# Performance work log

Hardware: AMD Instinct MI355X
Metric: run time of the kernel (lower is better)

The kernel has to match this reference:

```python
import jax, jax.numpy as jnp
import numpy as np

N, E, D, H = 16000, 256000, 128, 4
ALPHA = 0.2  # LeakyReLU negative slope


def setup_inputs() -> dict:
    key = jax.random.key(0)
    ks = jax.random.split(key, 9)
    s = 0.1
    return {
        "h": jax.random.normal(ks[0], (N, D), jnp.float32),
        "W": jax.random.normal(ks[1], (H, D, D), jnp.float32) * s,
        "a": jax.random.normal(ks[2], (H, 2 * D), jnp.float32) * s,
        "W_ih": jax.random.normal(ks[3], (3 * D, H * D), jnp.float32) * s,
        "W_hh": jax.random.normal(ks[4], (3 * D, D), jnp.float32) * s,
        "b_ih": jnp.zeros((3 * D,), jnp.float32),
        "b_hh": jnp.zeros((3 * D,), jnp.float32),
        "src": jax.random.randint(ks[5], (E,), 0, N, jnp.int32),
        "dst": jax.random.randint(ks[6], (E,), 0, N, jnp.int32),
    }


def reference(h, W, a, W_ih, W_hh, b_ih, b_hh, src, dst):
    n = h.shape[0]
    # Per-head linear transform: Wh[n,h,d]
    Wh = jnp.einsum("nd,hde->nhe", h, W)
    a1, a2 = a[:, :D], a[:, D:]
    s_src = jnp.einsum("nhd,hd->nh", Wh, a1)  # src attention logits
    s_dst = jnp.einsum("nhd,hd->nh", Wh, a2)  # dst attention logits
    e = jax.nn.leaky_relu(s_src[src] + s_dst[dst], ALPHA)  # [E,H]
    # Segment softmax over incoming edges of each dst node
    m = jax.ops.segment_max(e, dst, num_segments=n)          # [N,H]
    ex = jnp.exp(e - m[dst])
    denom = jax.ops.segment_sum(ex, dst, num_segments=n)     # [N,H]
    att = ex / denom[dst]                                    # [E,H]
    # Weighted message aggregation: h_prime[n,h,d]
    h_prime = jax.ops.segment_sum(att[:, :, None] * Wh[src], dst, num_segments=n)
    x = h_prime.reshape(n, H * D)  # concat heads
    # PyTorch GRUCell(input=H*D, hidden=D)
    gi = x @ W_ih.T + b_ih
    gh = h @ W_hh.T + b_hh
    i_r, i_z, i_n = jnp.split(gi, 3, axis=1)
    h_r, h_z, h_n = jnp.split(gh, 3, axis=1)
    r = jax.nn.sigmoid(i_r + h_r)
    z = jax.nn.sigmoid(i_z + h_z)
    nvec = jnp.tanh(i_n + r * h_n)
    return (1.0 - z) * nvec + z * h
```

## Files before the change

### kernel.cpp

```cpp
#include <hip/hip_runtime.h>
#include <math.h>

#define N_NODES 16000
#define E_EDGES 256000
#define DIM 128
#define HEADS 4
#define LRELU_ALPHA 0.2f
#define SLOT 64

typedef unsigned short u16;
typedef unsigned int u32;
typedef short bf16x8 __attribute__((ext_vector_type(8)));
typedef float floatx4 __attribute__((ext_vector_type(4)));

#define AS1 __attribute__((address_space(1)))
#define AS3 __attribute__((address_space(3)))

__device__ __forceinline__ u16 f2bf(float f) {
    u32 u = __float_as_uint(f);
    u32 r = (u + 0x7fffu + ((u >> 16) & 1u)) >> 16;
    return (u16)r;
}
__device__ __forceinline__ float bflo(u32 v) { return __uint_as_float(v << 16); }
__device__ __forceinline__ float bfhi(u32 v) { return __uint_as_float(v & 0xffff0000u); }
__device__ __forceinline__ u32 pack2(float lo, float hi) {
    return (u32)f2bf(lo) | ((u32)f2bf(hi) << 16);
}

__global__ __launch_bounds__(256) void prep_kernel(
    const float* __restrict__ W, const float* __restrict__ a,
    const float* __restrict__ W_ih, const float* __restrict__ W_hh,
    const int* __restrict__ src, const int* __restrict__ dst,
    u16* __restrict__ Wihb, u16* __restrict__ Wb,
    u16* __restrict__ Wcat, float* __restrict__ wa1, float* __restrict__ wa2,
    u32* __restrict__ cnt, int* __restrict__ ssort)
{
    const int b = blockIdx.x;
    const int tid = threadIdx.x;
    if (b < 1000) {
        int e = b * 256 + tid;
        u32 base = cnt[N_NODES];
        int d = dst[e];
        u32 pos = atomicAdd(&cnt[d], 1u) - base;
        ssort[d * SLOT + pos] = src[e];
    } else if (b < 1768) {
        int i = (b - 1000) * 256 + tid;
        Wihb[i] = f2bf(W_ih[i]);
        if (i < HEADS * DIM * DIM) Wb[i] = f2bf(W[i]);
    } else if (b < 1960) {
        int t = (b - 1768) * 256 + tid;
        int jp = t >> 7, e = t & 127;
        int j = (jp < 256) ? jp : jp + 128;
        Wcat[(size_t)j * 640 + 512 + e] = f2bf(W_hh[jp * 128 + e]);
    } else {
        int t = (b - 1960) * 256 + tid;
        int h = t >> 7;
        const float* wrow = W + (long)t * DIM;
        const float* a1 = a + h * 2 * DIM;
        const float* a2 = a1 + DIM;
        float s1 = 0.f, s2 = 0.f;
        for (int e = 0; e < DIM; ++e) {
            float w = wrow[e];
            s1 = fmaf(w, a1[e], s1);
            s2 = fmaf(w, a2[e], s2);
        }
        wa1[t] = s1;
        wa2[t] = s2;
    }
}

__device__ __forceinline__ void score_wave(int n, const float* __restrict__ hin,
    const float* __restrict__ wa1, const float* __restrict__ wa2,
    float* __restrict__ s_src, float* __restrict__ s_dst, u16* __restrict__ xcat, int lane)
{
    float2 hv = ((const float2*)hin)[n * 64 + lane];
    ((u32*)xcat)[n * 320 + 256 + lane] = pack2(hv.x, hv.y);
    float ps[4], qs[4];
    #pragma unroll
    for (int h = 0; h < 4; ++h) {
        float2 w1 = ((const float2*)(wa1 + h * 128))[lane];
        float2 w2 = ((const float2*)(wa2 + h * 128))[lane];
        float p = hv.x * w1.x + hv.y * w1.y;
        float q = hv.x * w2.x + hv.y * w2.y;
        #pragma unroll
        for (int off = 32; off > 0; off >>= 1) {
            p += __shfl_xor(p, off, 64);
            q += __shfl_xor(q, off, 64);
        }
        ps[h] = p; qs[h] = q;
    }
    if (lane == 0) {
        #pragma unroll
        for (int h = 0; h < 4; ++h) {
            s_src[n * HEADS + h] = ps[h];
            s_dst[n * HEADS + h] = qs[h];
        }
    }
}

__device__ __forceinline__ void gemm_tile(const u16* A, const u16* Bt, u16* C,
    int kstart, int kend, int lda, int ldb, int ldc, int row0, int col0, char* SMp, int tid)
{
    u16 (*Alds)[32] = (u16(*)[32])SMp;
    u16 (*Blds)[32] = (u16(*)[32])(SMp + 8192);
    const int wave = tid >> 6;
    const int lane = tid & 63;
    const int quad = lane >> 4;
    const int l15  = lane & 15;
    const int wm = (wave >> 1) * 64;
    const int wn = (wave & 1) * 64;
    const int ch0 = wave * 2;
    const int srow = lane >> 2;
    const int scol = (lane & 3) * 8;

    floatx4 acc[4][4] = {};

    for (int k0 = kstart; k0 < kend; k0 += 32) {
        #pragma unroll
        for (int c = 0; c < 2; ++c) {
            int ch = ch0 + c;
            const u16* ga = A + (size_t)(row0 + ch * 16 + srow) * lda + k0 + scol;
            __builtin_amdgcn_global_load_lds((AS1 void*)ga, (AS3 void*)&Alds[ch * 16][0], 16, 0, 0);
            const u16* gb = Bt + (size_t)(col0 + ch * 16 + srow) * ldb + k0 + scol;
            __builtin_amdgcn_global_load_lds((AS1 void*)gb, (AS3 void*)&Blds[ch * 16][0], 16, 0, 0);
        }
        __syncthreads();
        bf16x8 af[4], bfr[4];
        #pragma unroll
        for (int i = 0; i < 4; ++i) af[i] = *(const bf16x8*)&Alds[wm + i * 16 + l15][quad * 8];
        #pragma unroll
        for (int j = 0; j < 4; ++j) bfr[j] = *(const bf16x8*)&Blds[wn + j * 16 + l15][quad * 8];
        #pragma unroll
        for (int i = 0; i < 4; ++i)
            #pragma unroll
            for (int j = 0; j < 4; ++j)
                acc[i][j] = __builtin_amdgcn_mfma_f32_16x16x32_bf16(af[i], bfr[j], acc[i][j], 0, 0, 0);
        __syncthreads();
    }
    #pragma unroll
    for (int i = 0; i < 4; ++i) {
        #pragma unroll
        for (int r = 0; r < 4; ++r) {
            int row = row0 + wm + i * 16 + quad * 4 + r;
            size_t base = (size_t)row * ldc + col0 + wn + l15;
            #pragma unroll
            for (int j = 0; j < 4; ++j) C[base + j * 16] = f2bf(acc[i][j][r]);
        }
    }
}

__global__ __launch_bounds__(256) void mt_scores_kernel(
    const u16* __restrict__ Wihb, const u16* __restrict__ Wb, u16* __restrict__ Wcat,
    const float* __restrict__ hin, const float* __restrict__ wa1, const float* __restrict__ wa2,
    float* __restrict__ s_src, float* __restrict__ s_dst, u16* __restrict__ xcat)
{
    __shared__ __align__(16) char SM[16384];
    const int tid = threadIdx.x;
    const int b = blockIdx.x;
    if (b < 12) {
        int y = b % 3, z = b / 3;
        gemm_tile(Wihb + z * 128, Wb + (size_t)z * 16384, Wcat + z * 128,
                  0, 128, 512, 128, 640, y * 128, 0, SM, tid);
    } else {
        for (int n = (b - 12) * 4 + (tid >> 6); n < N_NODES; n += 1024 * 4)
            score_wave(n, hin, wa1, wa2, s_src, s_dst, xcat, tid & 63);
    }
}

__global__ __launch_bounds__(256) void aggregate_kernel(
    const float* __restrict__ s_src, const float* __restrict__ s_dst,
    const u32* __restrict__ cnt, const int* __restrict__ srcs,
    u16* __restrict__ xcat)
{
    const int tid = threadIdx.x;
    const int lane = tid & 63;
    const int n = blockIdx.x * 4 + (tid >> 6);
    const u32 base = cnt[N_NODES];
    const int deg = (int)(cnt[n] - base);
    const int start = n * SLOT;
    u32* xrow = (u32*)(xcat + (size_t)n * 640);
    if (deg == 0) {
        #pragma unroll
        for (int h = 0; h < 4; ++h) xrow[h * 64 + lane] = 0u;
        return;
    }
    const u32* hb = (const u32*)xcat;
    const float sd = s_dst[n * HEADS + (lane & 3)];
    const int j16 = lane >> 2;
    const int hh  = lane & 3;

    float2 acc[4] = {{0.f,0.f},{0.f,0.f},{0.f,0.f},{0.f,0.f}};
    float dsum[4] = {0.f, 0.f, 0.f, 0.f};

    for (int cb = 0; cb < deg; cb += 16) {
        const int clen = min(16, deg - cb);
        int sv = 0;
        if (lane < clen) sv = srcs[start + cb + lane];
        float wv = 0.f;
        if (j16 < clen) {
            int s = __shfl(sv, j16, 64);
            float e = s_src[s * HEADS + hh] + sd;
            e = e > 0.f ? e : LRELU_ALPHA * e;
            wv = __expf(e);
        }
        int e = 0;
        for (; e + 8 <= clen; e += 8) {
            u32 vs[8];
            #pragma unroll
            for (int k = 0; k < 8; ++k) {
                int s = __shfl(sv, e + k, 64);
                vs[k] = hb[s * 320 + 256 + lane];
            }
            #pragma unroll
            for (int k = 0; k < 8; ++k) {
                float lo = bflo(vs[k]), hi = bfhi(vs[k]);
                #pragma unroll
                for (int h = 0; h < 4; ++h) {
                    float w = __shfl(wv, (e + k) * 4 + h, 64);
                    acc[h].x = fmaf(w, lo, acc[h].x);
                    acc[h].y = fmaf(w, hi, acc[h].y);
                    dsum[h] += w;
                }
            }
        }
        for (; e < clen; ++e) {
            int s = __shfl(sv, e, 64);
            u32 v = hb[s * 320 + 256 + lane];
            float lo = bflo(v), hi = bfhi(v);
            #pragma unroll
            for (int h = 0; h < 4; ++h) {
                float w = __shfl(wv, e * 4 + h, 64);
                acc[h].x = fmaf(w, lo, acc[h].x);
                acc[h].y = fmaf(w, hi, acc[h].y);
                dsum[h] += w;
            }
        }
    }
    #pragma unroll
    for (int h = 0; h < 4; ++h) {
        float invd = 1.f / dsum[h];
        xrow[h * 64 + lane] = pack2(acc[h].x * invd, acc[h].y * invd);
    }
}

__global__ __launch_bounds__(256) void gemm_main_kernel(
    const u16* __restrict__ xcat, const u16* __restrict__ Wcat, u16* __restrict__ g)
{
    __shared__ __align__(16) char SM[16384];
    const int x = blockIdx.x;
    const int ks0 = (x == 3) ? 512 : 0;
    const int ke0 = (x == 2) ? 512 : 640;
    const int mid = (ks0 + ke0) >> 1;
    const int ks = blockIdx.z ? mid : ks0;
    const int ke = blockIdx.z ? ke0 : mid;
    u16* gp = g + (size_t)blockIdx.z * N_NODES * 512;
    gemm_tile(xcat, Wcat, gp, ks, ke, 640, 640, 512,
              blockIdx.y * 128, x * 128, SM, threadIdx.x);
}

__global__ __launch_bounds__(256) void gru_kernel(const u32* __restrict__ g32,
    const float* __restrict__ b_ih, const float* __restrict__ b_hh,
    const float* __restrict__ hin, float* __restrict__ out)
{
    int p = blockIdx.x * 256 + threadIdx.x;
    if (p >= N_NODES * 64) return;
    int n = p >> 6, d2 = p & 63;
    const u32* gr0 = g32 + (size_t)n * 256;
    const u32* gr1 = gr0 + (size_t)N_NODES * 256;
    u32 ar = gr0[d2],       br = gr1[d2];
    u32 az = gr0[64 + d2],  bz = gr1[64 + d2];
    u32 ai = gr0[128 + d2], bi = gr1[128 + d2];
    u32 ah = gr0[192 + d2], bh = gr1[192 + d2];
    const float2* bi2 = (const float2*)b_ih;
    const float2* bh2 = (const float2*)b_hh;
    float2 bir = bi2[d2],       bhr = bh2[d2];
    float2 biz = bi2[64 + d2],  bhz = bh2[64 + d2];
    float2 bin = bi2[128 + d2], bhn = bh2[128 + d2];
    float2 hv = ((const float2*)hin)[p];
    float2 o;
    {
        float A = bflo(ar) + bflo(br) + bir.x + bhr.x;
        float B = bflo(az) + bflo(bz) + biz.x + bhz.x;
        float Cn = bflo(ai) + bflo(bi) + bin.x;
        float Dn = bflo(ah) + bflo(bh) + bhn.x;
        float r = 1.f / (1.f + __expf(-A));
        float z = 1.f / (1.f + __expf(-B));
        float e2 = __expf(2.f * (Cn + r * Dn));
        float nv = (e2 - 1.f) / (e2 + 1.f);
        o.x = (1.f - z) * nv + z * hv.x;
    }
    {
        float A = bfhi(ar) + bfhi(br) + bir.y + bhr.y;
        float B = bfhi(az) + bfhi(bz) + biz.y + bhz.y;
        float Cn = bfhi(ai) + bfhi(bi) + bin.y;
        float Dn = bfhi(ah) + bfhi(bh) + bhn.y;
        float r = 1.f / (1.f + __expf(-A));
        float z = 1.f / (1.f + __expf(-B));
        float e2 = __expf(2.f * (Cn + r * Dn));
        float nv = (e2 - 1.f) / (e2 + 1.f);
        o.y = (1.f - z) * nv + z * hv.y;
    }
    ((float2*)out)[p] = o;
}

extern "C" void kernel_launch(void* const* d_in, const int* in_sizes, int n_in,
                              void* d_out, int out_size, void* d_ws, size_t ws_size,
                              hipStream_t stream)
{
    const float* h    = (const float*)d_in[0];
    const float* W    = (const float*)d_in[1];
    const float* a    = (const float*)d_in[2];
    const float* W_ih = (const float*)d_in[3];
    const float* W_hh = (const float*)d_in[4];
    const float* b_ih = (const float*)d_in[5];
    const float* b_hh = (const float*)d_in[6];
    const int*   src  = (const int*)d_in[7];
    const int*   dst  = (const int*)d_in[8];
    float* out = (float*)d_out;

    char* ws = (char*)d_ws;
    size_t off = 0;
    auto alloc = [&](size_t bytes) { void* p = ws + off; off += (bytes + 255) & ~(size_t)255; return p; };

    u16*   xcat = (u16*)alloc((size_t)N_NODES * 640 * 2);
    u16*   g    = (u16*)alloc((size_t)N_NODES * 512 * 2 * 2);
    u16*   Wihb = (u16*)alloc(384 * 512 * 2);
    u16*   Wb   = (u16*)alloc(HEADS * DIM * DIM * 2);
    u16*   Wcat = (u16*)alloc(512 * 640 * 2);
    float* wa1  = (float*)alloc(512 * 4);
    float* wa2  = (float*)alloc(512 * 4);
    float* s_src = (float*)alloc((size_t)N_NODES * HEADS * 4);
    float* s_dst = (float*)alloc((size_t)N_NODES * HEADS * 4);
    u32*   cnt  = (u32*)alloc((N_NODES + 1) * 4);
    int*   ssort = (int*)alloc((size_t)N_NODES * SLOT * 4);

    prep_kernel<<<1962, 256, 0, stream>>>(
        W, a, W_ih, W_hh, src, dst, Wihb, Wb, Wcat, wa1, wa2, cnt, ssort);

    mt_scores_kernel<<<1036, 256, 0, stream>>>(
        Wihb, Wb, Wcat, h, wa1, wa2, s_src, s_dst, xcat);

    aggregate_kernel<<<N_NODES / 4, 256, 0, stream>>>(s_src, s_dst, cnt, ssort, xcat);

    gemm_main_kernel<<<dim3(4, 125, 2), 256, 0, stream>>>(xcat, Wcat, g);

    gru_kernel<<<(N_NODES * 64 + 255) / 256, 256, 0, stream>>>(
        (const u32*)g, b_ih, b_hh, h, out);
}
```

Before: 153.4 us.

## Fuse final GEMM with GRU epilogue via gate-interleaved weight layout

Reorders the output columns of the concatenated weight so that each 128-column tile holds the r, z, i_n and h_n gates for 32 hidden dims, interleaved. The combined r/z gate sums now accumulate in a single K=640 pass, with zeroed blocks keeping the n-gate input and hidden parts separate. The GEMM is then fused with the GRU nonlinearity through an LDS-staged epilogue. This removes the bf16 intermediate g buffer (two split-K halves), its write and re-read, and one kernel launch. In exchange the grid drops from 1000 to 500 blocks, each doing the full K loop, and the output stores are 4-byte per thread.

```diff
diff --git a/kernel.cpp b/kernel.cpp
--- a/kernel.cpp
+++ b/kernel.cpp
@@ -23,9 +23,11 @@
 }
 __device__ __forceinline__ float bflo(u32 v) { return __uint_as_float(v << 16); }
 __device__ __forceinline__ float bfhi(u32 v) { return __uint_as_float(v & 0xffff0000u); }
+__device__ __forceinline__ float bfs(u16 v) { return __uint_as_float((u32)v << 16); }
 __device__ __forceinline__ u32 pack2(float lo, float hi) {
     return (u32)f2bf(lo) | ((u32)f2bf(hi) << 16);
 }
+
 
 __global__ __launch_bounds__(256) void prep_kernel(
     const float* __restrict__ W, const float* __restrict__ a,
@@ -50,10 +52,22 @@
     } else if (b < 1960) {
         int t = (b - 1768) * 256 + tid;
         int jp = t >> 7, e = t & 127;
-        int j = (jp < 256) ? jp : jp + 128;
-        Wcat[(size_t)j * 640 + 512 + e] = f2bf(W_hh[jp * 128 + e]);
+        int gate = jp >> 7;
+        if (gate == 2) gate = 3;
+        int p = (jp & 127) * 4 + gate;
+        Wcat[(size_t)p * 640 + 512 + e] = f2bf(W_hh[jp * 128 + e]);
+    } else if (b < 2280) {
+        int t = (b - 1960) * 256 + tid;
+        if (t < 16384) {
+            int d = t >> 7, e = t & 127;
+            Wcat[(size_t)(d * 4 + 2) * 640 + 512 + e] = 0;
+        } else {
+            int t2 = t - 16384;
+            int d = t2 >> 9, c = t2 & 511;
+            Wcat[(size_t)(d * 4 + 3) * 640 + c] = 0;
+        }
     } else {
-        int t = (b - 1960) * 256 + tid;
+        int t = (b - 2280) * 256 + tid;
         int h = t >> 7;
         const float* wrow = W + (long)t * DIM;
         const float* a1 = a + h * 2 * DIM;
@@ -98,6 +112,7 @@
     }
 }
 
+template<int PERM_C>
 __device__ __forceinline__ void gemm_tile(const u16* A, const u16* Bt, u16* C,
     int kstart, int kend, int lda, int ldb, int ldc, int row0, int col0, char* SMp, int tid)
 {
@@ -142,6 +157,7 @@
         #pragma unroll
         for (int r = 0; r < 4; ++r) {
             int row = row0 + wm + i * 16 + quad * 4 + r;
+            if (PERM_C) row = (row & 127) * 4 + (row >> 7);
             size_t base = (size_t)row * ldc + col0 + wn + l15;
             #pragma unroll
             for (int j = 0; j < 4; ++j) C[base + j * 16] = f2bf(acc[i][j][r]);
@@ -159,8 +175,8 @@
     const int b = blockIdx.x;
     if (b < 12) {
         int y = b % 3, z = b / 3;
-        gemm_tile(Wihb + z * 128, Wb + (size_t)z * 16384, Wcat + z * 128,
-                  0, 128, 512, 128, 640, y * 128, 0, SM, tid);
+        gemm_tile<1>(Wihb + z * 128, Wb + (size_t)z * 16384, Wcat + z * 128,
+                     0, 128, 512, 128, 640, y * 128, 0, SM, tid);
     } else {
         for (int n = (b - 12) * 4 + (tid >> 6); n < N_NODES; n += 1024 * 4)
             score_wave(n, hin, wa1, wa2, s_src, s_dst, xcat, tid & 63);
@@ -243,64 +259,83 @@
     }
 }
 
-__global__ __launch_bounds__(256) void gemm_main_kernel(
-    const u16* __restrict__ xcat, const u16* __restrict__ Wcat, u16* __restrict__ g)
-{
-    __shared__ __align__(16) char SM[16384];
-    const int x = blockIdx.x;
-    const int ks0 = (x == 3) ? 512 : 0;
-    const int ke0 = (x == 2) ? 512 : 640;
-    const int mid = (ks0 + ke0) >> 1;
-    const int ks = blockIdx.z ? mid : ks0;
-    const int ke = blockIdx.z ? ke0 : mid;
-    u16* gp = g + (size_t)blockIdx.z * N_NODES * 512;
-    gemm_tile(xcat, Wcat, gp, ks, ke, 640, 640, 512,
-              blockIdx.y * 128, x * 128, SM, threadIdx.x);
-}
-
-__global__ __launch_bounds__(256) void gru_kernel(const u32* __restrict__ g32,
+__global__ __launch_bounds__(256) void gemm_gru_kernel(
+    const u16* __restrict__ xcat, const u16* __restrict__ Wcat,
     const float* __restrict__ b_ih, const float* __restrict__ b_hh,
     const float* __restrict__ hin, float* __restrict__ out)
 {
-    int p = blockIdx.x * 256 + threadIdx.x;
-    if (p >= N_NODES * 64) return;
-    int n = p >> 6, d2 = p & 63;
-    const u32* gr0 = g32 + (size_t)n * 256;
-    const u32* gr1 = gr0 + (size_t)N_NODES * 256;
-    u32 ar = gr0[d2],       br = gr1[d2];
-    u32 az = gr0[64 + d2],  bz = gr1[64 + d2];
-    u32 ai = gr0[128 + d2], bi = gr1[128 + d2];
-    u32 ah = gr0[192 + d2], bh = gr1[192 + d2];
-    const float2* bi2 = (const float2*)b_ih;
-    const float2* bh2 = (const float2*)b_hh;
-    float2 bir = bi2[d2],       bhr = bh2[d2];
-    float2 biz = bi2[64 + d2],  bhz = bh2[64 + d2];
-    float2 bin = bi2[128 + d2], bhn = bh2[128 + d2];
-    float2 hv = ((const float2*)hin)[p];
-    float2 o;
-    {
-        float A = bflo(ar) + bflo(br) + bir.x + bhr.x;
-        float B = bflo(az) + bflo(bz) + biz.x + bhz.x;
-        float Cn = bflo(ai) + bflo(bi) + bin.x;
-        float Dn = bflo(ah) + bflo(bh) + bhn.x;
+    __shared__ __align__(16) char SM[32768];
+    u16 (*Alds)[32] = (u16(*)[32])SM;
+    u16 (*Blds)[32] = (u16(*)[32])(SM + 8192);
+    u16 (*tile)[128] = (u16(*)[128])SM;
+    const int tid = threadIdx.x;
+    const int wave = tid >> 6;
+    const int lane = tid & 63;
+    const int quad = lane >> 4;
+    const int l15  = lane & 15;
+    const int row0 = blockIdx.y * 128;
+    const int col0 = blockIdx.x * 128;
+    const int wm = (wave >> 1) * 64;
+    const int wn = (wave & 1) * 64;
+    const int ch0 = wave * 2;
+    const int srow = lane >> 2;
+    const int scol = (lane & 3) * 8;
+
+    floatx4 acc[4][4] = {};
+
+    for (int k0 = 0; k0 < 640; k0 += 32) {
+        #pragma unroll
+        for (int c = 0; c < 2; ++c) {
+            int ch = ch0 + c;
+            const u16* ga = xcat + (size_t)(row0 + ch * 16 + srow) * 640 + k0 + scol;
+            __builtin_amdgcn_global_load_lds((AS1 void*)ga, (AS3 void*)&Alds[ch * 16][0], 16, 0, 0);
+            const u16* gb = Wcat + (size_t)(col0 + ch * 16 + srow) * 640 + k0 + scol;
+            __builtin_amdgcn_global_load_lds((AS1 void*)gb, (AS3 void*)&Blds[ch * 16][0], 16, 0, 0);
+        }
+        __syncthreads();
+        bf16x8 af[4], bfr[4];
+        #pragma unroll
+        for (int i = 0; i < 4; ++i) af[i] = *(const bf16x8*)&Alds[wm + i * 16 + l15][quad * 8];
+        #pragma unroll
+        for (int j = 0; j < 4; ++j) bfr[j] = *(const bf16x8*)&Blds[wn + j * 16 + l15][quad * 8];
+        #pragma unroll
+        for (int i = 0; i < 4; ++i)
+            #pragma unroll
+            for (int j = 0; j < 4; ++j)
+                acc[i][j] = __builtin_amdgcn_mfma_f32_16x16x32_bf16(af[i], bfr[j], acc[i][j], 0, 0, 0);
+        __syncthreads();
+    }
+    #pragma unroll
+    for (int i = 0; i < 4; ++i)
+        #pragma unroll
+        for (int r = 0; r < 4; ++r) {
+            int row = wm + i * 16 + quad * 4 + r;
+            #pragma unroll
+            for (int j = 0; j < 4; ++j)
+                tile[row][wn + j * 16 + l15] = f2bf(acc[i][j][r]);
+        }
+    __syncthreads();
+    const int dim_l = tid & 31;
+    const int rg = tid >> 5;
+    const int dim_g = col0 / 4 + dim_l;
+    const float bir = b_ih[dim_g],       bhr = b_hh[dim_g];
+    const float biz = b_ih[128 + dim_g], bhz = b_hh[128 + dim_g];
+    const float bin = b_ih[256 + dim_g], bhn = b_hh[256 + dim_g];
+    #pragma unroll
+    for (int i = 0; i < 16; ++i) {
+        int row = rg * 16 + i;
+        int node = row0 + row;
+        ushort4 gv = *(const ushort4*)&tile[row][dim_l * 4];
+        float A  = bfs(gv.x) + bir + bhr;
+        float B  = bfs(gv.y) + biz + bhz;
+        float Cn = bfs(gv.z) + bin;
+        float Dn = bfs(gv.w) + bhn;
         float r = 1.f / (1.f + __expf(-A));
         float z = 1.f / (1.f + __expf(-B));
         float e2 = __expf(2.f * (Cn + r * Dn));
         float nv = (e2 - 1.f) / (e2 + 1.f);
-        o.x = (1.f - z) * nv + z * hv.x;
-    }
-    {
-        float A = bfhi(ar) + bfhi(br) + bir.y + bhr.y;
-        float B = bfhi(az) + bfhi(bz) + biz.y + bhz.y;
-        float Cn = bfhi(ai) + bfhi(bi) + bin.y;
-        float Dn = bfhi(ah) + bfhi(bh) + bhn.y;
-        float r = 1.f / (1.f + __expf(-A));
-        float z = 1.f / (1.f + __expf(-B));
-        float e2 = __expf(2.f * (Cn + r * Dn));
-        float nv = (e2 - 1.f) / (e2 + 1.f);
-        o.y = (1.f - z) * nv + z * hv.y;
-    }
-    ((float2*)out)[p] = o;
+        out[(size_t)node * 128 + dim_g] = (1.f - z) * nv + z * hin[(size_t)node * 128 + dim_g];
+    }
 }
 
 extern "C" void kernel_launch(void* const* d_in, const int* in_sizes, int n_in,
@@ -323,7 +358,6 @@
     auto alloc = [&](size_t bytes) { void* p = ws + off; off += (bytes + 255) & ~(size_t)255; return p; };
 
     u16*   xcat = (u16*)alloc((size_t)N_NODES * 640 * 2);
-    u16*   g    = (u16*)alloc((size_t)N_NODES * 512 * 2 * 2);
     u16*   Wihb = (u16*)alloc(384 * 512 * 2);
     u16*   Wb   = (u16*)alloc(HEADS * DIM * DIM * 2);
     u16*   Wcat = (u16*)alloc(512 * 640 * 2);
@@ -334,7 +368,7 @@
     u32*   cnt  = (u32*)alloc((N_NODES + 1) * 4);
     int*   ssort = (int*)alloc((size_t)N_NODES * SLOT * 4);
 
-    prep_kernel<<<1962, 256, 0, stream>>>(
+    prep_kernel<<<2282, 256, 0, stream>>>(
         W, a, W_ih, W_hh, src, dst, Wihb, Wb, Wcat, wa1, wa2, cnt, ssort);
 
     mt_scores_kernel<<<1036, 256, 0, stream>>>(
@@ -342,8 +376,5 @@
 
     aggregate_kernel<<<N_NODES / 4, 256, 0, stream>>>(s_src, s_dst, cnt, ssort, xcat);
 
-    gemm_main_kernel<<<dim3(4, 125, 2), 256, 0, stream>>>(xcat, Wcat, g);
-
-    gru_kernel<<<(N_NODES * 64 + 255) / 256, 256, 0, stream>>>(
-        (const u32*)g, b_ih, b_hh, h, out);
-}
+    gemm_gru_kernel<<<dim3(4, 125), 256, 0, stream>>>(xcat, Wcat, b_ih, b_hh, h, out);
+}
```

New measurement: 145.4 us. 5.2% less time.
